# Performance work log

Hardware: AMD Instinct MI355X
Metric: run time of the kernel (lower is better)

## Reference

```python
import jax, jax.numpy as jnp
import numpy as np
import math

B, S, H, NH, K = 1, 4096, 1024, 16, 32
HD = H // NH


def setup_inputs() -> dict:
    key = jax.random.key(0)
    ks = jax.random.split(key, 8)
    x = jax.random.normal(ks[0], (B, S, H), dtype=jnp.float32)
    # per-query top-K indices; make them causal (idx[q] <= q) so every row has >=1 valid key
    idx_raw = jax.random.randint(ks[1], (S, K), 0, S)
    idx = idx_raw % (jnp.arange(S)[:, None] + 1)
    valid = jnp.ones((S, K), dtype=bool)
    geo_bias = jax.random.normal(ks[2], (NH, S, K), dtype=jnp.float32)
    scale = 1.0 / math.sqrt(H)
    Wq = jax.random.normal(ks[3], (H, H), dtype=jnp.float32) * scale
    Wk = jax.random.normal(ks[4], (H, H), dtype=jnp.float32) * scale
    Wv = jax.random.normal(ks[5], (H, H), dtype=jnp.float32) * scale
    Wo = jax.random.normal(ks[6], (H, H), dtype=jnp.float32) * scale
    bo = jnp.zeros((H,), dtype=jnp.float32)
    return {"x": x, "idx": idx, "valid": valid, "geo_bias": geo_bias,
            "Wq": Wq, "Wk": Wk, "Wv": Wv, "Wo": Wo, "bo": bo}


def reference(x, idx, valid, geo_bias, Wq, Wk, Wv, Wo, bo):
    b, s, h = x.shape
    nh = geo_bias.shape[0]
    hd = h // nh
    kk = idx.shape[1]
    # projections -> [b, nh, s, hd]
    def proj(W):
        return (x @ W).reshape(b, s, nh, hd).transpose(0, 2, 1, 3)
    q, k, v = proj(Wq), proj(Wk), proj(Wv)
    # gather per-query selected keys/values: [b, nh, s, K, hd]
    k_sel = k[:, :, idx]
    v_sel = v[:, :, idx]
    # scores via elementwise mult + reduce over head_dim
    logits = jnp.einsum('bhsd,bhskd->bhsk', q, k_sel) / math.sqrt(hd)
    logits = logits + geo_bias[None]
    mask = valid & (idx <= jnp.arange(s)[:, None])  # [s, K]
    logits = jnp.where(mask[None, None], logits, jnp.float32(-1e30))
    attn = jax.nn.softmax(logits, axis=-1)
    out = jnp.einsum('bhsk,bhskd->bhsd', attn, v_sel)
    out = out.transpose(0, 2, 1, 3).reshape(b, s, h)
    return out @ Wo + bo
```

## Files before the change

kernel.cpp:

```cpp
#include <hip/hip_runtime.h>
#include <hip/hip_bf16.h>
#include <stdint.h>

typedef unsigned short u16;
typedef __attribute__((ext_vector_type(8))) short bf16x8;
typedef __attribute__((ext_vector_type(4))) float f32x4;
typedef __attribute__((ext_vector_type(2))) float f32x2;

typedef const __attribute__((address_space(1))) unsigned int* gptr_t;
typedef __attribute__((address_space(3))) unsigned int* lptr_t;

__device__ __forceinline__ float bf2f(u16 v) {
    unsigned int u = ((unsigned int)v) << 16;
    float f;
    __builtin_memcpy(&f, &u, 4);
    return f;
}
__device__ __forceinline__ u16 f2bf(float f) {
    unsigned int u;
    __builtin_memcpy(&u, &f, 4);
    u += 0x7FFFu + ((u >> 16) & 1u);
    return (u16)(u >> 16);
}
__device__ __forceinline__ float bflo(unsigned int u) {
    unsigned int x = u << 16; float f; __builtin_memcpy(&f, &x, 4); return f;
}
__device__ __forceinline__ float bfhi(unsigned int u) {
    unsigned int x = u & 0xFFFF0000u; float f; __builtin_memcpy(&f, &x, 4); return f;
}
__device__ __forceinline__ f32x2 upk(unsigned int u) {
    return (f32x2){bflo(u), bfhi(u)};
}

#define BM 128
#define BN 128
#define BK 32

__global__ __launch_bounds__(256) void gemm_bk64(const u16* __restrict__ A,
                                                 const u16* __restrict__ Bt,
                                                 u16* __restrict__ C,
                                                 int M, int N, int K) {
    __shared__ u16 As[BM * 64];
    __shared__ u16 Bs[BN * 64];

    const int t    = threadIdx.x;
    const int lane = t & 63;
    const int wave = t >> 6;
    const int wm   = (wave >> 1) * 64;
    const int wn   = (wave & 1) * 64;
    const int m0   = blockIdx.y * BM;
    const int n0   = blockIdx.x * BN;

    const int r5   = t >> 3;
    const int pc   = t & 7;
    const int lc   = pc ^ (r5 & 7);

    const int quad = lane >> 4;
    const int l16  = lane & 15;
    const int sw   = l16 & 7;

    f32x4 acc[4][4];
#pragma unroll
    for (int i = 0; i < 4; i++)
#pragma unroll
        for (int j = 0; j < 4; j++) acc[i][j] = (f32x4){0.f, 0.f, 0.f, 0.f};

    for (int k0 = 0; k0 < K; k0 += 64) {
#pragma unroll
        for (int p = 0; p < 4; p++) {
            const u16* ga = A  + (size_t)(m0 + r5 + 32 * p) * K + k0 + lc * 8;
            const u16* gb = Bt + (size_t)(n0 + r5 + 32 * p) * K + k0 + lc * 8;
            __builtin_amdgcn_global_load_lds((gptr_t)ga, (lptr_t)(&As[t * 8 + p * 2048]), 16, 0, 0);
            __builtin_amdgcn_global_load_lds((gptr_t)gb, (lptr_t)(&Bs[t * 8 + p * 2048]), 16, 0, 0);
        }
        __syncthreads();

#pragma unroll
        for (int k2 = 0; k2 < 2; k2++) {
            bf16x8 af[4], bfg[4];
#pragma unroll
            for (int i = 0; i < 4; i++)
                af[i] = *(const bf16x8*)&As[(wm + i * 16 + l16) * 64 + ((k2 * 4 + quad) ^ sw) * 8];
#pragma unroll
            for (int j = 0; j < 4; j++)
                bfg[j] = *(const bf16x8*)&Bs[(wn + j * 16 + l16) * 64 + ((k2 * 4 + quad) ^ sw) * 8];
#pragma unroll
            for (int i = 0; i < 4; i++)
#pragma unroll
                for (int j = 0; j < 4; j++)
                    acc[i][j] = __builtin_amdgcn_mfma_f32_16x16x32_bf16(af[i], bfg[j], acc[i][j], 0, 0, 0);
        }
        __syncthreads();
    }

#pragma unroll
    for (int j = 0; j < 4; j++) {
        const int n = n0 + wn + j * 16 + l16;
#pragma unroll
        for (int i = 0; i < 4; i++) {
            const int mbase = m0 + wm + i * 16 + quad * 4;
#pragma unroll
            for (int r = 0; r < 4; r++)
                C[(size_t)(mbase + r) * N + n] = f2bf(acc[i][j][r]);
        }
    }
}

__global__ __launch_bounds__(512) void gemm_bt_w8(const u16* __restrict__ A,
                                                  const u16* __restrict__ Bt,
                                                  float* __restrict__ C,
                                                  const float* __restrict__ bias,
                                                  int M, int N, int K) {
    __shared__ u16 As[BM * BK];
    __shared__ u16 Bs[BN * BK];

    const int t    = threadIdx.x;
    const int lane = t & 63;
    const int wave = t >> 6;
    const int wm   = (wave >> 2) * 64;
    const int wn   = (wave & 3) * 32;
    const int m0   = blockIdx.y * BM;
    const int n0   = blockIdx.x * BN;

    const int row  = t >> 2;
    const int kcol = (t & 3) * 8;

    const int quad = lane >> 4;
    const int l16  = lane & 15;

    f32x4 acc[4][2];
#pragma unroll
    for (int i = 0; i < 4; i++)
#pragma unroll
        for (int j = 0; j < 2; j++) acc[i][j] = (f32x4){0.f, 0.f, 0.f, 0.f};

    for (int k0 = 0; k0 < K; k0 += BK) {
        const u16* ga = A  + (size_t)(m0 + row) * K + k0 + kcol;
        const u16* gb = Bt + (size_t)(n0 + row) * K + k0 + kcol;
        __builtin_amdgcn_global_load_lds((gptr_t)ga, (lptr_t)(&As[t * 8]), 16, 0, 0);
        __builtin_amdgcn_global_load_lds((gptr_t)gb, (lptr_t)(&Bs[t * 8]), 16, 0, 0);
        __syncthreads();

        bf16x8 af[4], bfg[2];
#pragma unroll
        for (int i = 0; i < 4; i++)
            af[i] = *(const bf16x8*)&As[(wm + i * 16 + l16) * BK + quad * 8];
#pragma unroll
        for (int j = 0; j < 2; j++)
            bfg[j] = *(const bf16x8*)&Bs[(wn + j * 16 + l16) * BK + quad * 8];

#pragma unroll
        for (int i = 0; i < 4; i++)
#pragma unroll
            for (int j = 0; j < 2; j++)
                acc[i][j] = __builtin_amdgcn_mfma_f32_16x16x32_bf16(af[i], bfg[j], acc[i][j], 0, 0, 0);
        __syncthreads();
    }

#pragma unroll
    for (int j = 0; j < 2; j++) {
        const int n  = n0 + wn + j * 16 + l16;
        const float bv = bias ? bias[n] : 0.f;
#pragma unroll
        for (int i = 0; i < 4; i++) {
            const int mbase = m0 + wm + i * 16 + quad * 4;
#pragma unroll
            for (int r = 0; r < 4; r++)
                C[(size_t)(mbase + r) * N + n] = acc[i][j][r] + bv;
        }
    }
}

__global__ __launch_bounds__(256) void prep_k(const float* __restrict__ x,
                                              const float* __restrict__ W0,
                                              const float* __restrict__ W1,
                                              const float* __restrict__ W2,
                                              const float* __restrict__ W3,
                                              u16* __restrict__ x_bf,
                                              u16* __restrict__ Dqkv,
                                              u16* __restrict__ Do) {
    const int b = blockIdx.x;
    if (b < 4096) {
        const int i = b * 256 + threadIdx.x;
        const float4 v = ((const float4*)x)[i];
        u16 o[4] = {f2bf(v.x), f2bf(v.y), f2bf(v.z), f2bf(v.w)};
        *(uint64_t*)&x_bf[i * 4] = *(uint64_t*)o;
        return;
    }
    __shared__ u16 tile[32][33];
    const int bb  = b - 4096;
    const int z   = bb >> 10;
    const int t10 = bb & 1023;
    const int c0  = (t10 & 31) * 32;
    const int r0  = (t10 >> 5) * 32;
    const float* src = (z == 0) ? W0 : (z == 1) ? W1 : (z == 2) ? W2 : W3;
    u16* dst = (z < 3) ? (Dqkv + (size_t)z * 1024 * 1024) : Do;
    const int tx = threadIdx.x & 31;
    const int ty = threadIdx.x >> 5;
#pragma unroll
    for (int i = 0; i < 32; i += 8)
        tile[ty + i][tx] = f2bf(src[(size_t)(r0 + ty + i) * 1024 + c0 + tx]);
    __syncthreads();
#pragma unroll
    for (int i = 0; i < 32; i += 8)
        dst[(size_t)(c0 + ty + i) * 1024 + r0 + tx] = tile[tx][ty + i];
}

__global__ __launch_bounds__(256, 8) void attn_k(const u16* __restrict__ QKV,
                                                 const int* __restrict__ idx,
                                                 const float* __restrict__ geo,
                                                 u16* __restrict__ AO) {
    __shared__ float dot_lds[4 * 64];
    __shared__ float w_lds[4 * 64];

    const int t    = threadIdx.x;
    const int lane = t & 63;
    const int wave = t >> 6;
    const int b    = blockIdx.x;
    const int hp   = b & 7;
    const int s    = ((b >> 3) << 2) + wave;
    const int h0   = hp * 2;
    const int hsel = lane >> 5;
    const int kk   = lane & 31;
    const int g    = lane >> 3;
    const int c8   = lane & 7;

    const char* qb = (const char*)QKV;

    const int j    = idx[s * 32 + kk];
    const int joff = j * 6144;

    const uint4 qA = *(const uint4*)(qb + (size_t)s * 6144 + h0 * 128 + c8 * 16);
    const uint4 qB = *(const uint4*)(qb + (size_t)s * 6144 + h0 * 128 + 128 + c8 * 16);
    const f32x2 qa0 = upk(qA.x), qa1 = upk(qA.y), qa2 = upk(qA.z), qa3 = upk(qA.w);
    const f32x2 qb0 = upk(qB.x), qb1 = upk(qB.y), qb2 = upk(qB.z), qb3 = upk(qB.w);

#pragma unroll
    for (int i = 0; i < 8; i++) {
        const int rh = i * 8 + g;
        const int jm = __shfl(j, rh & 31);
        const uint4 kv = *(const uint4*)(qb + (size_t)(unsigned)(jm * 6144) + 2048 +
                                         (h0 + (i >> 2)) * 128 + c8 * 16);
        f32x2 d2;
        if (i < 4) {
            d2  = upk(kv.x) * qa0;
            d2 += upk(kv.y) * qa1;
            d2 += upk(kv.z) * qa2;
            d2 += upk(kv.w) * qa3;
        } else {
            d2  = upk(kv.x) * qb0;
            d2 += upk(kv.y) * qb1;
            d2 += upk(kv.z) * qb2;
            d2 += upk(kv.w) * qb3;
        }
        float d = d2.x + d2.y;
        d += __shfl_xor(d, 1);
        d += __shfl_xor(d, 2);
        d += __shfl_xor(d, 4);
        if (c8 == 0) dot_lds[wave * 64 + rh] = d;
    }

    float lg2 = dot_lds[wave * 64 + lane] * 0.125f +
                geo[((size_t)(h0 + hsel) * 4096 + s) * 32 + kk];
    if (j > s) lg2 = -1e30f;

    float mx = lg2;
    mx = fmaxf(mx, __shfl_xor(mx, 16));
    mx = fmaxf(mx, __shfl_xor(mx, 8));
    mx = fmaxf(mx, __shfl_xor(mx, 4));
    mx = fmaxf(mx, __shfl_xor(mx, 2));
    mx = fmaxf(mx, __shfl_xor(mx, 1));
    const float p = __expf(lg2 - mx);
    float sum = p;
    sum += __shfl_xor(sum, 16);
    sum += __shfl_xor(sum, 8);
    sum += __shfl_xor(sum, 4);
    sum += __shfl_xor(sum, 2);
    sum += __shfl_xor(sum, 1);
    const float w = p / sum;
    w_lds[wave * 64 + lane] = w;

    const int half = lane >> 5;
    const int e8   = lane & 31;
    const int vconst = 4096 + h0 * 128 + 8 * e8;
    const int whead  = (e8 >> 4) * 32;
    f32x4 av = (f32x4){0.f, 0.f, 0.f, 0.f};
#pragma unroll
    for (int i = 0; i < 16; i++) {
        const int   jo = __shfl(joff, 2 * i + half);
        const float wq = w_lds[wave * 64 + whead + 2 * i + half];
        const uint2 vv = *(const uint2*)(qb + (size_t)(unsigned)jo + vconst);
        const f32x2 v01 = upk(vv.x), v23 = upk(vv.y);
        av.x += wq * v01.x;
        av.y += wq * v01.y;
        av.z += wq * v23.x;
        av.w += wq * v23.y;
    }
    av.x += __shfl_xor(av.x, 32);
    av.y += __shfl_xor(av.y, 32);
    av.z += __shfl_xor(av.z, 32);
    av.w += __shfl_xor(av.w, 32);
    if (lane < 32) {
        u16 o[4] = {f2bf(av.x), f2bf(av.y), f2bf(av.z), f2bf(av.w)};
        *(uint2*)&AO[(size_t)s * 1024 + h0 * 64 + 4 * lane] = *(uint2*)o;
    }
}

extern "C" void kernel_launch(void* const* d_in, const int* in_sizes, int n_in,
                              void* d_out, int out_size, void* d_ws, size_t ws_size,
                              hipStream_t stream) {
    const float* x   = (const float*)d_in[0];
    const int*   idx = (const int*)d_in[1];
    const float* geo = (const float*)d_in[3];
    const float* Wq  = (const float*)d_in[4];
    const float* Wk  = (const float*)d_in[5];
    const float* Wv  = (const float*)d_in[6];
    const float* Wo  = (const float*)d_in[7];
    const float* bo  = (const float*)d_in[8];
    float* out = (float*)d_out;

    u16* x_bf   = (u16*)d_ws;
    u16* wt_qkv = x_bf + (size_t)4096 * 1024;
    u16* wt_o   = wt_qkv + (size_t)3 * 1024 * 1024;
    u16* qkv    = wt_o + (size_t)1024 * 1024;
    u16* ao     = qkv + (size_t)4096 * 3072;

    const dim3 tb(256);
    prep_k<<<dim3(8192), tb, 0, stream>>>(x, Wq, Wk, Wv, Wo, x_bf, wt_qkv, wt_o);

    gemm_bk64<<<dim3(3072 / BN, 4096 / BM), tb, 0, stream>>>(
        x_bf, wt_qkv, qkv, 4096, 3072, 1024);
    attn_k<<<dim3(4096 * 8 / 4), tb, 0, stream>>>(qkv, idx, geo, ao);
    gemm_bt_w8<<<dim3(1024 / BN, 4096 / BM), dim3(512), 0, stream>>>(
        ao, wt_o, out, bo, 4096, 1024, 1024);
}
```

Measured before the change: 183.8 us.

## Prefetch all K/V gathers up front in attention and retile output GEMM

The attention kernel now issues every K and V gather load into registers before any arithmetic, separated by a sched barrier, and replaces the LDS staging of dot products and softmax weights with wave shuffles. Issuing the gathers together lets their latencies overlap instead of stalling on each one. The occupancy hint is lowered from 8 to 5 to make room for the larger register footprint. The output projection GEMM moves to 128x64 tiles with BK=64, 256 threads and XOR-swizzled LDS, which doubles the block count and reduces bank conflicts, at the cost of a different balance between loads and MFMA work.

```diff
diff --git a/kernel.cpp b/kernel.cpp
--- a/kernel.cpp
+++ b/kernel.cpp
@@ -34,7 +34,6 @@
 
 #define BM 128
 #define BN 128
-#define BK 32
 
 __global__ __launch_bounds__(256) void gemm_bk64(const u16* __restrict__ A,
                                                  const u16* __restrict__ Bt,
@@ -106,27 +105,29 @@
     }
 }
 
-__global__ __launch_bounds__(512) void gemm_bt_w8(const u16* __restrict__ A,
-                                                  const u16* __restrict__ Bt,
-                                                  float* __restrict__ C,
-                                                  const float* __restrict__ bias,
-                                                  int M, int N, int K) {
-    __shared__ u16 As[BM * BK];
-    __shared__ u16 Bs[BN * BK];
+__global__ __launch_bounds__(256) void gemm_o(const u16* __restrict__ A,
+                                              const u16* __restrict__ Bt,
+                                              float* __restrict__ C,
+                                              const float* __restrict__ bias,
+                                              int M, int N, int K) {
+    __shared__ u16 As[128 * 64];
+    __shared__ u16 Bs[64 * 64];
 
     const int t    = threadIdx.x;
     const int lane = t & 63;
     const int wave = t >> 6;
-    const int wm   = (wave >> 2) * 64;
-    const int wn   = (wave & 3) * 32;
-    const int m0   = blockIdx.y * BM;
-    const int n0   = blockIdx.x * BN;
-
-    const int row  = t >> 2;
-    const int kcol = (t & 3) * 8;
+    const int wm   = (wave >> 1) * 64;
+    const int wn   = (wave & 1) * 32;
+    const int m0   = blockIdx.y * 128;
+    const int n0   = blockIdx.x * 64;
+
+    const int r5   = t >> 3;
+    const int pc   = t & 7;
+    const int lc   = pc ^ (r5 & 7);
 
     const int quad = lane >> 4;
     const int l16  = lane & 15;
+    const int sw   = l16 & 7;
 
     f32x4 acc[4][2];
 #pragma unroll
@@ -134,26 +135,34 @@
 #pragma unroll
         for (int j = 0; j < 2; j++) acc[i][j] = (f32x4){0.f, 0.f, 0.f, 0.f};
 
-    for (int k0 = 0; k0 < K; k0 += BK) {
-        const u16* ga = A  + (size_t)(m0 + row) * K + k0 + kcol;
-        const u16* gb = Bt + (size_t)(n0 + row) * K + k0 + kcol;
-        __builtin_amdgcn_global_load_lds((gptr_t)ga, (lptr_t)(&As[t * 8]), 16, 0, 0);
-        __builtin_amdgcn_global_load_lds((gptr_t)gb, (lptr_t)(&Bs[t * 8]), 16, 0, 0);
+    for (int k0 = 0; k0 < K; k0 += 64) {
+#pragma unroll
+        for (int p = 0; p < 4; p++) {
+            const u16* ga = A + (size_t)(m0 + r5 + 32 * p) * K + k0 + lc * 8;
+            __builtin_amdgcn_global_load_lds((gptr_t)ga, (lptr_t)(&As[t * 8 + p * 2048]), 16, 0, 0);
+        }
+#pragma unroll
+        for (int p = 0; p < 2; p++) {
+            const u16* gb = Bt + (size_t)(n0 + r5 + 32 * p) * K + k0 + lc * 8;
+            __builtin_amdgcn_global_load_lds((gptr_t)gb, (lptr_t)(&Bs[t * 8 + p * 2048]), 16, 0, 0);
+        }
         __syncthreads();
 
-        bf16x8 af[4], bfg[2];
-#pragma unroll
-        for (int i = 0; i < 4; i++)
-            af[i] = *(const bf16x8*)&As[(wm + i * 16 + l16) * BK + quad * 8];
-#pragma unroll
-        for (int j = 0; j < 2; j++)
-            bfg[j] = *(const bf16x8*)&Bs[(wn + j * 16 + l16) * BK + quad * 8];
-
-#pragma unroll
-        for (int i = 0; i < 4; i++)
+#pragma unroll
+        for (int k2 = 0; k2 < 2; k2++) {
+            bf16x8 af[4], bfg[2];
+#pragma unroll
+            for (int i = 0; i < 4; i++)
+                af[i] = *(const bf16x8*)&As[(wm + i * 16 + l16) * 64 + ((k2 * 4 + quad) ^ sw) * 8];
 #pragma unroll
             for (int j = 0; j < 2; j++)
-                acc[i][j] = __builtin_amdgcn_mfma_f32_16x16x32_bf16(af[i], bfg[j], acc[i][j], 0, 0, 0);
+                bfg[j] = *(const bf16x8*)&Bs[(wn + j * 16 + l16) * 64 + ((k2 * 4 + quad) ^ sw) * 8];
+#pragma unroll
+            for (int i = 0; i < 4; i++)
+#pragma unroll
+                for (int j = 0; j < 2; j++)
+                    acc[i][j] = __builtin_amdgcn_mfma_f32_16x16x32_bf16(af[i], bfg[j], acc[i][j], 0, 0, 0);
+        }
         __syncthreads();
     }
 
@@ -206,13 +215,10 @@
         dst[(size_t)(c0 + ty + i) * 1024 + r0 + tx] = tile[tx][ty + i];
 }
 
-__global__ __launch_bounds__(256, 8) void attn_k(const u16* __restrict__ QKV,
+__global__ __launch_bounds__(256, 5) void attn_k(const u16* __restrict__ QKV,
                                                  const int* __restrict__ idx,
                                                  const float* __restrict__ geo,
                                                  u16* __restrict__ AO) {
-    __shared__ float dot_lds[4 * 64];
-    __shared__ float w_lds[4 * 64];
-
     const int t    = threadIdx.x;
     const int lane = t & 63;
     const int wave = t >> 6;
@@ -227,41 +233,60 @@
 
     const char* qb = (const char*)QKV;
 
+    const float gv = geo[((size_t)(h0 + hsel) * 4096 + s) * 32 + kk];
     const int j    = idx[s * 32 + kk];
     const int joff = j * 6144;
 
     const uint4 qA = *(const uint4*)(qb + (size_t)s * 6144 + h0 * 128 + c8 * 16);
     const uint4 qB = *(const uint4*)(qb + (size_t)s * 6144 + h0 * 128 + 128 + c8 * 16);
-    const f32x2 qa0 = upk(qA.x), qa1 = upk(qA.y), qa2 = upk(qA.z), qa3 = upk(qA.w);
-    const f32x2 qb0 = upk(qB.x), qb1 = upk(qB.y), qb2 = upk(qB.z), qb3 = upk(qB.w);
-
+
+    uint4 kreg[8];
 #pragma unroll
     for (int i = 0; i < 8; i++) {
         const int rh = i * 8 + g;
         const int jm = __shfl(j, rh & 31);
-        const uint4 kv = *(const uint4*)(qb + (size_t)(unsigned)(jm * 6144) + 2048 +
-                                         (h0 + (i >> 2)) * 128 + c8 * 16);
+        kreg[i] = *(const uint4*)(qb + (size_t)(unsigned)(jm * 6144) + 2048 +
+                                  (h0 + (i >> 2)) * 128 + c8 * 16);
+    }
+
+    const int half = lane >> 5;
+    const int e8   = lane & 31;
+    const int vconst = 4096 + h0 * 128 + 8 * e8;
+    uint2 vreg[16];
+#pragma unroll
+    for (int i = 0; i < 16; i++) {
+        const int jo = __shfl(joff, 2 * i + half);
+        vreg[i] = *(const uint2*)(qb + (size_t)(unsigned)jo + vconst);
+    }
+    __builtin_amdgcn_sched_barrier(0);
+
+    const f32x2 qa0 = upk(qA.x), qa1 = upk(qA.y), qa2 = upk(qA.z), qa3 = upk(qA.w);
+    const f32x2 qb0 = upk(qB.x), qb1 = upk(qB.y), qb2 = upk(qB.z), qb3 = upk(qB.w);
+
+    float mydot = 0.f;
+#pragma unroll
+    for (int i = 0; i < 8; i++) {
         f32x2 d2;
         if (i < 4) {
-            d2  = upk(kv.x) * qa0;
-            d2 += upk(kv.y) * qa1;
-            d2 += upk(kv.z) * qa2;
-            d2 += upk(kv.w) * qa3;
+            d2  = upk(kreg[i].x) * qa0;
+            d2 += upk(kreg[i].y) * qa1;
+            d2 += upk(kreg[i].z) * qa2;
+            d2 += upk(kreg[i].w) * qa3;
         } else {
-            d2  = upk(kv.x) * qb0;
-            d2 += upk(kv.y) * qb1;
-            d2 += upk(kv.z) * qb2;
-            d2 += upk(kv.w) * qb3;
+            d2  = upk(kreg[i].x) * qb0;
+            d2 += upk(kreg[i].y) * qb1;
+            d2 += upk(kreg[i].z) * qb2;
+            d2 += upk(kreg[i].w) * qb3;
         }
         float d = d2.x + d2.y;
         d += __shfl_xor(d, 1);
         d += __shfl_xor(d, 2);
         d += __shfl_xor(d, 4);
-        if (c8 == 0) dot_lds[wave * 64 + rh] = d;
-    }
-
-    float lg2 = dot_lds[wave * 64 + lane] * 0.125f +
-                geo[((size_t)(h0 + hsel) * 4096 + s) * 32 + kk];
+        const float dsel = __shfl(d, (lane & 7) << 3);
+        mydot = ((lane >> 3) == i) ? dsel : mydot;
+    }
+
+    float lg2 = mydot * 0.125f + gv;
     if (j > s) lg2 = -1e30f;
 
     float mx = lg2;
@@ -278,19 +303,13 @@
     sum += __shfl_xor(sum, 2);
     sum += __shfl_xor(sum, 1);
     const float w = p / sum;
-    w_lds[wave * 64 + lane] = w;
-
-    const int half = lane >> 5;
-    const int e8   = lane & 31;
-    const int vconst = 4096 + h0 * 128 + 8 * e8;
-    const int whead  = (e8 >> 4) * 32;
+
+    const int whead = (e8 >> 4) * 32;
     f32x4 av = (f32x4){0.f, 0.f, 0.f, 0.f};
 #pragma unroll
     for (int i = 0; i < 16; i++) {
-        const int   jo = __shfl(joff, 2 * i + half);
-        const float wq = w_lds[wave * 64 + whead + 2 * i + half];
-        const uint2 vv = *(const uint2*)(qb + (size_t)(unsigned)jo + vconst);
-        const f32x2 v01 = upk(vv.x), v23 = upk(vv.y);
+        const float wq = __shfl(w, whead + 2 * i + half);
+        const f32x2 v01 = upk(vreg[i].x), v23 = upk(vreg[i].y);
         av.x += wq * v01.x;
         av.y += wq * v01.y;
         av.z += wq * v23.x;
@@ -331,6 +350,6 @@
     gemm_bk64<<<dim3(3072 / BN, 4096 / BM), tb, 0, stream>>>(
         x_bf, wt_qkv, qkv, 4096, 3072, 1024);
     attn_k<<<dim3(4096 * 8 / 4), tb, 0, stream>>>(qkv, idx, geo, ao);
-    gemm_bt_w8<<<dim3(1024 / BN, 4096 / BM), dim3(512), 0, stream>>>(
+    gemm_o<<<dim3(1024 / 64, 4096 / 128), tb, 0, stream>>>(
         ao, wt_o, out, bo, 4096, 1024, 1024);
 }
```

Measured after the change: 181.1 us. No clear change (-1.5%).
